# Kernel tuning notes

Measured on AMD Instinct MI355X. Metric: run time of the kernel, lower is better.

The kernel has to match this reference:

```python
import jax, jax.numpy as jnp
import numpy as np

B, S, D, H = 2, 2048, 1024, 16
HD = D // H  # 64


def setup_inputs() -> dict:
    key = jax.random.key(0)
    ks = jax.random.split(key, 9)
    sd = 1.0 / np.sqrt(D)  # torch Linear default init scale (uniform, but normal ok for ref)
    return {
        "x": jax.random.normal(ks[0], (B, S, D), dtype=jnp.float32),
        # torch Linear weight is [out, in]; stack per head -> [H, HD, D]
        "Wq": jax.random.normal(ks[1], (H, HD, D), dtype=jnp.float32) * sd,
        "bq": jax.random.normal(ks[2], (H, HD), dtype=jnp.float32) * sd,
        "Wk": jax.random.normal(ks[3], (H, HD, D), dtype=jnp.float32) * sd,
        "bk": jax.random.normal(ks[4], (H, HD), dtype=jnp.float32) * sd,
        "Wv": jax.random.normal(ks[5], (H, HD, D), dtype=jnp.float32) * sd,
        "bv": jax.random.normal(ks[6], (H, HD), dtype=jnp.float32) * sd,
        "Wp": jax.random.normal(ks[7], (D, D), dtype=jnp.float32) * sd,
        "bp": jax.random.normal(ks[8], (D,), dtype=jnp.float32) * sd,
    }


def reference(x, Wq, bq, Wk, bk, Wv, bv, Wp, bp):
    # Per-head QKV projections, batched over heads: [B,S,D] x [H,HD,D] -> [B,H,S,HD]
    q = jnp.einsum("bsd,hed->bhse", x, Wq) + bq[None, :, None, :]
    k = jnp.einsum("bsd,hed->bhse", x, Wk) + bk[None, :, None, :]
    v = jnp.einsum("bsd,hed->bhse", x, Wv) + bv[None, :, None, :]
    scale = 1.0 / np.sqrt(HD)
    scores = jnp.einsum("bhse,bhte->bhst", q, k) * scale  # [B,H,S,S]
    attn = jax.nn.softmax(scores, axis=-1)
    out = jnp.einsum("bhst,bhte->bhse", attn, v)  # [B,H,S,HD]
    # concat heads along last dim (head-major order matches torch.cat over heads)
    out = out.transpose(0, 2, 1, 3).reshape(x.shape[0], x.shape[1], -1)  # [B,S,D]
    return out @ Wp.T + bp
```

## Files before the change

kernel.cpp:

```cpp
#include <hip/hip_runtime.h>
#include <hip/hip_bf16.h>
#include <stdint.h>

#define B_  2
#define S_  2048
#define D_  1024
#define H_  16
#define HD_ 64
#define M_  (B_*S_)
#define BH_ (B_*H_)

typedef __bf16 bf16;
typedef bf16  bf16x8 __attribute__((ext_vector_type(8)));
typedef bf16  bf16x4 __attribute__((ext_vector_type(4)));
typedef bf16  bf16x2 __attribute__((ext_vector_type(2)));
typedef float f32x4  __attribute__((ext_vector_type(4)));

#define SCALE_LOG2E 0.18033688011112042f
#define MFIX_LOG2E  23.083120654223415f

__device__ __forceinline__ f32x4 mfma16(bf16x8 a, bf16x8 b, f32x4 c) {
    return __builtin_amdgcn_mfma_f32_16x16x32_bf16(a, b, c, 0, 0, 0);
}
__device__ __forceinline__ float fexp2(float x) {
    return __builtin_amdgcn_exp2f(x);
}

__device__ __forceinline__ void gload_lds16(const bf16* g, bf16* l) {
    auto* gp = reinterpret_cast<__attribute__((address_space(1))) uint32_t*>(
        reinterpret_cast<uintptr_t>(const_cast<bf16*>(g)));
    auto* lp = reinterpret_cast<__attribute__((address_space(3))) uint32_t*>(
        reinterpret_cast<uintptr_t>(l));
    __builtin_amdgcn_global_load_lds(gp, lp, 16, 0, 0);
}

__global__ __launch_bounds__(256) void k_convert(
        const float* __restrict__ x,
        const float* __restrict__ wq, const float* __restrict__ wk,
        const float* __restrict__ wv, const float* __restrict__ wp,
        bf16* __restrict__ xb,
        bf16* __restrict__ wqb, bf16* __restrict__ wkb,
        bf16* __restrict__ wvb, bf16* __restrict__ wpb) {
    const int y = blockIdx.y;
    const float* src = (y == 0) ? x : (y == 1) ? wq : (y == 2) ? wk
                     : (y == 3) ? wv : wp;
    bf16* dst        = (y == 0) ? xb : (y == 1) ? wqb : (y == 2) ? wkb
                     : (y == 3) ? wvb : wpb;
    const int reps = (y == 0) ? 4 : 1;
    const int idx = blockIdx.x * 256 + threadIdx.x;
    for (int rep = 0; rep < reps; ++rep) {
        const size_t e = (size_t)rep * (1u << 20) + (size_t)idx * 4;
        const float4 f = *(const float4*)(src + e);
        bf16x4 o;
        o[0] = (bf16)f.x; o[1] = (bf16)f.y; o[2] = (bf16)f.z; o[3] = (bf16)f.w;
        *(bf16x4*)(dst + e) = o;
    }
}

__global__ __launch_bounds__(256) void k_gemm_qkv(
        const bf16* __restrict__ x,
        const bf16* __restrict__ Wq, const bf16* __restrict__ Wk, const bf16* __restrict__ Wv,
        const float* __restrict__ bq, const float* __restrict__ bk, const float* __restrict__ bv,
        bf16* __restrict__ q, bf16* __restrict__ k, bf16* __restrict__ vt) {
    const int z = blockIdx.z;
    const bf16* A   = x;
    const bf16* Bt  = (z == 0) ? Wq : (z == 1) ? Wk : Wv;
    const float* bias = (z == 0) ? bq : (z == 1) ? bk : bv;
    bf16* C         = (z == 0) ? q  : (z == 1) ? k  : vt;
    const float sc  = (z == 0) ? SCALE_LOG2E : 1.0f;

    __shared__ bf16 As[128*32];
    __shared__ bf16 Bs[128*32];
    const int K = D_;
    const int tid = threadIdx.x;
    const int w  = tid >> 6, L = tid & 63;
    const int lr = L & 15,  lq = L >> 4;
    const int tileM = blockIdx.y * 128, tileN = blockIdx.x * 128;
    const int wm = (w >> 1) * 64, wn = (w & 1) * 64;

    const f32x4 fzero = {0.f, 0.f, 0.f, 0.f};
    f32x4 acc[4][4];
#pragma unroll
    for (int i = 0; i < 4; ++i)
#pragma unroll
        for (int j = 0; j < 4; ++j) acc[i][j] = fzero;

    const int srow   = L >> 2;
    const int schunk = (L & 3) ^ (srow & 3) ^ ((srow >> 2) & 3);
    const bf16* ag = A  + (size_t)(tileM + w*32 + srow) * K + schunk*8;
    const bf16* bg = Bt + (size_t)(tileN + w*32 + srow) * K + schunk*8;
    bf16* asd = &As[(w*32)*32];
    bf16* bsd = &Bs[(w*32)*32];
    const int sw = (lr & 3) ^ ((lr >> 2) & 3);

    for (int kt = 0; kt < K; kt += 32) {
        __syncthreads();
        gload_lds16(ag + kt,          asd);
        gload_lds16(ag + kt + 16*K,   asd + 16*32);
        gload_lds16(bg + kt,          bsd);
        gload_lds16(bg + kt + 16*K,   bsd + 16*32);
        __syncthreads();

        bf16x8 af[4], bfr[4];
#pragma unroll
        for (int i = 0; i < 4; ++i)
            af[i]  = *(const bf16x8*)&As[(wm + i*16 + lr)*32 + ((lq ^ sw) * 8)];
#pragma unroll
        for (int j = 0; j < 4; ++j)
            bfr[j] = *(const bf16x8*)&Bs[(wn + j*16 + lr)*32 + ((lq ^ sw) * 8)];
#pragma unroll
        for (int i = 0; i < 4; ++i)
#pragma unroll
            for (int j = 0; j < 4; ++j)
                acc[i][j] = mfma16(af[i], bfr[j], acc[i][j]);
    }

#pragma unroll
    for (int i = 0; i < 4; ++i) {
#pragma unroll
        for (int j = 0; j < 4; ++j) {
            const int m0 = tileM + wm + i*16 + lq*4;
            const int n  = tileN + wn + j*16 + lr;
            const int h = n >> 6, e = n & 63;
            if (z != 2) {
#pragma unroll
                for (int r = 0; r < 4; ++r) {
                    const int m = m0 + r;
                    const int b = m >> 11, s = m & (S_ - 1);
                    C[((size_t)((b*H_ + h)*S_ + s) << 6) + e] =
                        (bf16)((acc[i][j][r] + bias[n]) * sc);
                }
            } else {
                const int b = m0 >> 11, s0 = m0 & (S_ - 1);
                const int s0p = (s0 & ~31) | (lq*8) | ((i & 1)*4);
                const float bn = bias[n];
                bf16x4 t4;
#pragma unroll
                for (int r = 0; r < 4; ++r) t4[r] = (bf16)(acc[i][j][r] + bn);
                *(bf16x4*)&C[(((size_t)(b*H_ + h)*HD_ + e) << 11) + s0p] = t4;
            }
        }
    }
}

__global__ __launch_bounds__(256, 4) void k_gemm_proj(
        const bf16* __restrict__ A, const bf16* __restrict__ Bt,
        const float* __restrict__ bias, float* __restrict__ C) {
    __shared__ bf16 As[64*32];
    __shared__ bf16 Bs[128*32];
    const int K = D_;
    const int tid = threadIdx.x;
    const int w  = tid >> 6, L = tid & 63;
    const int lr = L & 15,  lq = L >> 4;
    const int tileM = blockIdx.y * 64, tileN = blockIdx.x * 128;
    const int wm = (w >> 1) * 32, wn = (w & 1) * 64;

    const f32x4 fzero = {0.f, 0.f, 0.f, 0.f};
    f32x4 acc[2][4];
#pragma unroll
    for (int i = 0; i < 2; ++i)
#pragma unroll
        for (int j = 0; j < 4; ++j) acc[i][j] = fzero;

    const int srow   = L >> 2;
    const int schunk = (L & 3) ^ (srow & 3) ^ ((srow >> 2) & 3);
    const bf16* ag = A  + (size_t)(tileM + w*16 + srow) * K + schunk*8;
    const bf16* bg = Bt + (size_t)(tileN + w*16 + srow) * K + schunk*8;
    bf16* asd = &As[(w*16)*32];
    bf16* bsd = &Bs[(w*16)*32];
    const int sw = (lr & 3) ^ ((lr >> 2) & 3);

    for (int kt = 0; kt < K; kt += 32) {
        __syncthreads();
        gload_lds16(ag + kt,          asd);
        gload_lds16(bg + kt,          bsd);
        gload_lds16(bg + kt + 64*K,   bsd + 64*32);
        __syncthreads();

        bf16x8 af[2], bfr[4];
#pragma unroll
        for (int i = 0; i < 2; ++i)
            af[i]  = *(const bf16x8*)&As[(wm + i*16 + lr)*32 + ((lq ^ sw) * 8)];
#pragma unroll
        for (int j = 0; j < 4; ++j)
            bfr[j] = *(const bf16x8*)&Bs[(wn + j*16 + lr)*32 + ((lq ^ sw) * 8)];
#pragma unroll
        for (int i = 0; i < 2; ++i)
#pragma unroll
            for (int j = 0; j < 4; ++j)
                acc[i][j] = mfma16(af[i], bfr[j], acc[i][j]);
    }

#pragma unroll
    for (int i = 0; i < 2; ++i) {
#pragma unroll
        for (int j = 0; j < 4; ++j) {
#pragma unroll
            for (int r = 0; r < 4; ++r) {
                const int m = tileM + wm + i*16 + lq*4 + r;
                const int n = tileN + wn + j*16 + lr;
                C[(size_t)m * D_ + n] = acc[i][j][r] + bias[n];
            }
        }
    }
}

__global__ __launch_bounds__(256, 2) void k_attn(const bf16* __restrict__ Q,
                                                 const bf16* __restrict__ Kg,
                                                 const bf16* __restrict__ Vt,
                                                 bf16* __restrict__ O) {
    __shared__ bf16 Ks[3][64*64];
    __shared__ bf16 Vs[3][64*64];
    const int tid = threadIdx.x;
    const int w  = tid >> 6, L = tid & 63;
    const int lr = L & 15,  lq = L >> 4;

    const int id = blockIdx.y * 16 + blockIdx.x;
    const int xcd = id & 7, g = id >> 3;
    const int bh   = xcd * 4 + (g >> 4);
    const int qblk = g & 15;
    const int q0 = qblk * 128 + w * 32;

    const size_t base = (size_t)bh * S_ * HD_;
    const bf16* qp = Q  + base;
    const bf16* kp = Kg + base;
    const bf16* vp = Vt + base;

    bf16x8 qf[2][2];
#pragma unroll
    for (int h2 = 0; h2 < 2; ++h2) {
        qf[h2][0] = *(const bf16x8*)&qp[(q0 + h2*16 + lr)*HD_ + lq*8];
        qf[h2][1] = *(const bf16x8*)&qp[(q0 + h2*16 + lr)*HD_ + 32 + lq*8];
    }

    const int rbase = (w & 1) * 32;
    const int srow  = L >> 3;
    const int gchunk = (L & 7) ^ srow;

    const int c0 = ((lq ^ (lr & 7))) * 8;
    const int c1 = ((lq ^ (lr & 7)) ^ 4) * 8;

    const f32x4 fzero = {0.f, 0.f, 0.f, 0.f};
    const f32x4 fmfix = {-MFIX_LOG2E, -MFIX_LOG2E, -MFIX_LOG2E, -MFIX_LOG2E};
    bf16x8 vones;
#pragma unroll
    for (int i = 0; i < 8; ++i) vones[i] = (bf16)1.0f;

    f32x4 acc_l[2] = {fzero, fzero};
    f32x4 o_acc[2][4];
#pragma unroll
    for (int h2 = 0; h2 < 2; ++h2)
#pragma unroll
        for (int eb = 0; eb < 4; ++eb) o_acc[h2][eb] = fzero;

#pragma unroll
    for (int t = 0; t < 2; ++t) {
        const int tb = t * 64;
        if (w < 2) {
#pragma unroll
            for (int i = 0; i < 4; ++i)
                gload_lds16(kp + (size_t)(tb + rbase + i*8 + srow)*HD_ + gchunk*8,
                            &Ks[t][(rbase + i*8)*HD_]);
        } else {
#pragma unroll
            for (int i = 0; i < 4; ++i)
                gload_lds16(vp + (size_t)(rbase + i*8 + srow)*S_ + tb + gchunk*8,
                            &Vs[t][(rbase + i*8)*HD_]);
        }
    }

    int cur = 0;
    for (int it = 0; it < S_/64; ++it) {
        if (it + 1 < S_/64) {
            asm volatile("s_waitcnt vmcnt(4)" ::: "memory");
        } else {
            asm volatile("s_waitcnt vmcnt(0)" ::: "memory");
        }
        __builtin_amdgcn_s_barrier();
        __builtin_amdgcn_sched_barrier(0);

        if (it + 2 < S_/64) {
            const int pbuf = (cur >= 1) ? cur - 1 : cur + 2;
            const int t2 = (it + 2) * 64;
            if (w < 2) {
#pragma unroll
                for (int i = 0; i < 4; ++i)
                    gload_lds16(kp + (size_t)(t2 + rbase + i*8 + srow)*HD_ + gchunk*8,
                                &Ks[pbuf][(rbase + i*8)*HD_]);
            } else {
#pragma unroll
                for (int i = 0; i < 4; ++i)
                    gload_lds16(vp + (size_t)(rbase + i*8 + srow)*S_ + t2 + gchunk*8,
                                &Vs[pbuf][(rbase + i*8)*HD_]);
            }
        }

        __builtin_amdgcn_s_setprio(1);

        bf16x4 d4[2][4];
#pragma unroll
        for (int j = 0; j < 4; ++j) {
            const bf16x8 kf0 = *(const bf16x8*)&Ks[cur][(j*16 + lr)*HD_ + c0];
            const bf16x8 kf1 = *(const bf16x8*)&Ks[cur][(j*16 + lr)*HD_ + c1];
#pragma unroll
            for (int h2 = 0; h2 < 2; ++h2) {
                f32x4 z = fmfix;
                z = mfma16(kf0, qf[h2][0], z);
                z = mfma16(kf1, qf[h2][1], z);
                bf16x4 t4;
#pragma unroll
                for (int r = 0; r < 4; ++r)
                    t4[r] = (bf16)fexp2(z[r]);
                d4[h2][j] = t4;
            }
        }

        bf16x8 pb[2][2];
#pragma unroll
        for (int h2 = 0; h2 < 2; ++h2) {
#pragma unroll
            for (int kh = 0; kh < 2; ++kh) {
                union { bf16x4 h[2]; bf16x8 v; } u;
                u.h[0] = d4[h2][2*kh + 0];
                u.h[1] = d4[h2][2*kh + 1];
                pb[h2][kh] = u.v;
            }
        }

#pragma unroll
        for (int h2 = 0; h2 < 2; ++h2) {
            acc_l[h2] = mfma16(vones, pb[h2][0], acc_l[h2]);
            acc_l[h2] = mfma16(vones, pb[h2][1], acc_l[h2]);
        }

#pragma unroll
        for (int eb = 0; eb < 4; ++eb) {
            const bf16x8 vb0 = *(const bf16x8*)&Vs[cur][(eb*16 + lr)*HD_ + c0];
            const bf16x8 vb1 = *(const bf16x8*)&Vs[cur][(eb*16 + lr)*HD_ + c1];
#pragma unroll
            for (int h2 = 0; h2 < 2; ++h2) {
                o_acc[h2][eb] = mfma16(vb0, pb[h2][0], o_acc[h2][eb]);
                o_acc[h2][eb] = mfma16(vb1, pb[h2][1], o_acc[h2][eb]);
            }
        }

        __builtin_amdgcn_s_setprio(0);

        cur = (cur == 2) ? 0 : cur + 1;
    }

    const int b = bh >> 4, h = bh & 15;
#pragma unroll
    for (int h2 = 0; h2 < 2; ++h2) {
        const float inv = 1.f / acc_l[h2][0];
        const size_t obase = ((size_t)(b*S_ + q0 + h2*16 + lr))*D_ + h*64;
#pragma unroll
        for (int eb = 0; eb < 4; ++eb)
#pragma unroll
            for (int b2 = 0; b2 < 2; ++b2) {
                bf16x2 t2 = { (bf16)(o_acc[h2][eb][2*b2]   * inv),
                              (bf16)(o_acc[h2][eb][2*b2+1] * inv) };
                *(bf16x2*)&O[obase + eb*16 + lq*4 + 2*b2] = t2;
            }
    }
}

extern "C" void kernel_launch(void* const* d_in, const int* in_sizes, int n_in,
                              void* d_out, int out_size, void* d_ws, size_t ws_size,
                              hipStream_t stream) {
    const float* x  = (const float*)d_in[0];
    const float* Wq = (const float*)d_in[1];
    const float* bq = (const float*)d_in[2];
    const float* Wk = (const float*)d_in[3];
    const float* bk = (const float*)d_in[4];
    const float* Wv = (const float*)d_in[5];
    const float* bv = (const float*)d_in[6];
    const float* Wp = (const float*)d_in[7];
    const float* bp = (const float*)d_in[8];
    float* out = (float*)d_out;

    const size_t NE = (size_t)B_ * H_ * S_ * HD_;
    const size_t NW = (size_t)D_ * D_;
    bf16* xb  = (bf16*)d_ws;
    bf16* wqb = xb + NE;
    bf16* wkb = wqb + NW;
    bf16* wvb = wkb + NW;
    bf16* wpb = wvb + NW;
    bf16* q_ws  = wpb + NW;
    bf16* k_ws  = q_ws + NE;
    bf16* vt_ws = k_ws + NE;
    bf16* a_ws  = xb;

    k_convert<<<dim3(1024, 5), 256, 0, stream>>>(x, Wq, Wk, Wv, Wp,
                                                 xb, wqb, wkb, wvb, wpb);
    k_gemm_qkv<<<dim3(D_/128, M_/128, 3), 256, 0, stream>>>(
        xb, wqb, wkb, wvb, bq, bk, bv, q_ws, k_ws, vt_ws);
    k_attn<<<dim3(S_/128, BH_), 256, 0, stream>>>(q_ws, k_ws, vt_ws, a_ws);
    k_gemm_proj<<<dim3(D_/128, M_/64), 256, 0, stream>>>(a_ws, wpb, bp, out);
}
```

Measured before the change: 181.2 us.

## Triple-buffer LDS in QKV and projection GEMMs with async prefetch two tiles ahead

Both GEMM kernels move from a single LDS buffer with two barriers per k-step to a three-stage ring buffer. Global-to-LDS loads for tile it+2 are issued while tile it is computed, and explicit vmcnt waits plus one barrier per iteration replace the double __syncthreads. This hides global load latency behind the MFMA work. It costs triple the shared memory, which may lower occupancy, and correctness depends on the hand-counted vmcnt values.

```diff
diff --git a/kernel.cpp b/kernel.cpp
--- a/kernel.cpp
+++ b/kernel.cpp
@@ -69,8 +69,8 @@
     bf16* C         = (z == 0) ? q  : (z == 1) ? k  : vt;
     const float sc  = (z == 0) ? SCALE_LOG2E : 1.0f;
 
-    __shared__ bf16 As[128*32];
-    __shared__ bf16 Bs[128*32];
+    __shared__ bf16 As[3][128*32];
+    __shared__ bf16 Bs[3][128*32];
     const int K = D_;
     const int tid = threadIdx.x;
     const int w  = tid >> 6, L = tid & 63;
@@ -89,30 +89,55 @@
     const int schunk = (L & 3) ^ (srow & 3) ^ ((srow >> 2) & 3);
     const bf16* ag = A  + (size_t)(tileM + w*32 + srow) * K + schunk*8;
     const bf16* bg = Bt + (size_t)(tileN + w*32 + srow) * K + schunk*8;
-    bf16* asd = &As[(w*32)*32];
-    bf16* bsd = &Bs[(w*32)*32];
+    const int soff = (w*32)*32;
     const int sw = (lr & 3) ^ ((lr >> 2) & 3);
 
-    for (int kt = 0; kt < K; kt += 32) {
-        __syncthreads();
-        gload_lds16(ag + kt,          asd);
-        gload_lds16(ag + kt + 16*K,   asd + 16*32);
-        gload_lds16(bg + kt,          bsd);
-        gload_lds16(bg + kt + 16*K,   bsd + 16*32);
-        __syncthreads();
+#pragma unroll
+    for (int t = 0; t < 2; ++t) {
+        bf16* asd = &As[t][soff];
+        bf16* bsd = &Bs[t][soff];
+        gload_lds16(ag + t*32,          asd);
+        gload_lds16(ag + t*32 + 16*K,   asd + 16*32);
+        gload_lds16(bg + t*32,          bsd);
+        gload_lds16(bg + t*32 + 16*K,   bsd + 16*32);
+    }
+
+    const int NIT = K / 32;
+    int cur = 0;
+    for (int it = 0; it < NIT; ++it) {
+        if (it + 1 < NIT) {
+            asm volatile("s_waitcnt vmcnt(4)" ::: "memory");
+        } else {
+            asm volatile("s_waitcnt vmcnt(0)" ::: "memory");
+        }
+        __builtin_amdgcn_s_barrier();
+        __builtin_amdgcn_sched_barrier(0);
+
+        if (it + 2 < NIT) {
+            const int pbuf = (cur >= 1) ? cur - 1 : 2;
+            const int kt2 = (it + 2) * 32;
+            bf16* asd = &As[pbuf][soff];
+            bf16* bsd = &Bs[pbuf][soff];
+            gload_lds16(ag + kt2,          asd);
+            gload_lds16(ag + kt2 + 16*K,   asd + 16*32);
+            gload_lds16(bg + kt2,          bsd);
+            gload_lds16(bg + kt2 + 16*K,   bsd + 16*32);
+        }
 
         bf16x8 af[4], bfr[4];
 #pragma unroll
         for (int i = 0; i < 4; ++i)
-            af[i]  = *(const bf16x8*)&As[(wm + i*16 + lr)*32 + ((lq ^ sw) * 8)];
+            af[i]  = *(const bf16x8*)&As[cur][(wm + i*16 + lr)*32 + ((lq ^ sw) * 8)];
 #pragma unroll
         for (int j = 0; j < 4; ++j)
-            bfr[j] = *(const bf16x8*)&Bs[(wn + j*16 + lr)*32 + ((lq ^ sw) * 8)];
+            bfr[j] = *(const bf16x8*)&Bs[cur][(wn + j*16 + lr)*32 + ((lq ^ sw) * 8)];
 #pragma unroll
         for (int i = 0; i < 4; ++i)
 #pragma unroll
             for (int j = 0; j < 4; ++j)
                 acc[i][j] = mfma16(af[i], bfr[j], acc[i][j]);
+
+        cur = (cur == 2) ? 0 : cur + 1;
     }
 
 #pragma unroll
@@ -146,8 +171,8 @@
 __global__ __launch_bounds__(256, 4) void k_gemm_proj(
         const bf16* __restrict__ A, const bf16* __restrict__ Bt,
         const float* __restrict__ bias, float* __restrict__ C) {
-    __shared__ bf16 As[64*32];
-    __shared__ bf16 Bs[128*32];
+    __shared__ bf16 As[3][64*32];
+    __shared__ bf16 Bs[3][128*32];
     const int K = D_;
     const int tid = threadIdx.x;
     const int w  = tid >> 6, L = tid & 63;
@@ -166,29 +191,53 @@
     const int schunk = (L & 3) ^ (srow & 3) ^ ((srow >> 2) & 3);
     const bf16* ag = A  + (size_t)(tileM + w*16 + srow) * K + schunk*8;
     const bf16* bg = Bt + (size_t)(tileN + w*16 + srow) * K + schunk*8;
-    bf16* asd = &As[(w*16)*32];
-    bf16* bsd = &Bs[(w*16)*32];
+    const int aoff = (w*16)*32;
     const int sw = (lr & 3) ^ ((lr >> 2) & 3);
 
-    for (int kt = 0; kt < K; kt += 32) {
-        __syncthreads();
-        gload_lds16(ag + kt,          asd);
-        gload_lds16(bg + kt,          bsd);
-        gload_lds16(bg + kt + 64*K,   bsd + 64*32);
-        __syncthreads();
+#pragma unroll
+    for (int t = 0; t < 2; ++t) {
+        bf16* asd = &As[t][aoff];
+        bf16* bsd = &Bs[t][aoff];
+        gload_lds16(ag + t*32,          asd);
+        gload_lds16(bg + t*32,          bsd);
+        gload_lds16(bg + t*32 + 64*K,   bsd + 64*32);
+    }
+
+    const int NIT = K / 32;
+    int cur = 0;
+    for (int it = 0; it < NIT; ++it) {
+        if (it + 1 < NIT) {
+            asm volatile("s_waitcnt vmcnt(3)" ::: "memory");
+        } else {
+            asm volatile("s_waitcnt vmcnt(0)" ::: "memory");
+        }
+        __builtin_amdgcn_s_barrier();
+        __builtin_amdgcn_sched_barrier(0);
+
+        if (it + 2 < NIT) {
+            const int pbuf = (cur >= 1) ? cur - 1 : 2;
+            const int kt2 = (it + 2) * 32;
+            bf16* asd = &As[pbuf][aoff];
+            bf16* bsd = &Bs[pbuf][aoff];
+            gload_lds16(ag + kt2,          asd);
+            gload_lds16(bg + kt2,          bsd);
+            gload_lds16(bg + kt2 + 64*K,   bsd + 64*32);
+        }
 
         bf16x8 af[2], bfr[4];
 #pragma unroll
         for (int i = 0; i < 2; ++i)
-            af[i]  = *(const bf16x8*)&As[(wm + i*16 + lr)*32 + ((lq ^ sw) * 8)];
+            af[i]  = *(const bf16x8*)&As[cur][(wm + i*16 + lr)*32 + ((lq ^ sw) * 8)];
 #pragma unroll
         for (int j = 0; j < 4; ++j)
-            bfr[j] = *(const bf16x8*)&Bs[(wn + j*16 + lr)*32 + ((lq ^ sw) * 8)];
+            bfr[j] = *(const bf16x8*)&Bs[cur][(wn + j*16 + lr)*32 + ((lq ^ sw) * 8)];
 #pragma unroll
         for (int i = 0; i < 2; ++i)
 #pragma unroll
             for (int j = 0; j < 4; ++j)
                 acc[i][j] = mfma16(af[i], bfr[j], acc[i][j]);
+
+        cur = (cur == 2) ? 0 : cur + 1;
     }
 
 #pragma unroll
```

Result: no change. 181.0 us (-0.1%).
